# Kernel tuning notes

Hardware: AMD Instinct MI355X
Metric: run time of the kernel (lower is better)

The kernel has to match this reference:

```python
import jax, jax.numpy as jnp
import numpy as np

N_NODES = 50000
N_EDGES = 800000
IN_DIM = 128
OUT_DIM = 128


def setup_inputs() -> dict:
    key = jax.random.key(0)
    k1, k2, k3, k4, k5 = jax.random.split(key, 5)
    x = jax.random.normal(k1, (N_NODES, IN_DIM), dtype=jnp.float32)
    # Xavier-uniform-ish scale for the two weight matrices
    scale = float(np.sqrt(6.0 / (IN_DIM + OUT_DIM)))
    Wg = jax.random.uniform(k2, (OUT_DIM, IN_DIM), dtype=jnp.float32, minval=-scale, maxval=scale)
    Wl = jax.random.uniform(k3, (OUT_DIM, IN_DIM), dtype=jnp.float32, minval=-scale, maxval=scale)
    bias = jnp.zeros((OUT_DIM,), dtype=jnp.float32)
    neigh_idx = jax.random.randint(k4, (N_EDGES,), 0, N_NODES, dtype=jnp.int32)
    seg_ids = jnp.sort(jax.random.randint(k5, (N_EDGES,), 0, N_NODES, dtype=jnp.int32))
    return {"x": x, "Wg": Wg, "Wl": Wl, "bias": bias,
            "neigh_idx": neigh_idx, "seg_ids": seg_ids}


def reference(x, Wg, Wl, bias, neigh_idx, seg_ids):
    N = x.shape[0]
    # global 1x1 map on all nodes (self path)
    global_maps = x @ Wg.T                                  # [N, out]
    # per-edge neighbor features: local + global maps of the neighbor
    neigh_x = x[neigh_idx]                                  # [E, in]
    mixed = neigh_x @ Wl.T + global_maps[neigh_idx]         # [E, out]
    # segment-mean over each destination node's neighbors
    sums = jax.ops.segment_sum(mixed, seg_ids, num_segments=N)            # [N, out]
    cnt = jax.ops.segment_sum(jnp.ones((seg_ids.shape[0],), x.dtype), seg_ids, num_segments=N)  # [N]
    mean = sums / jnp.maximum(cnt, 1.0)[:, None]
    # deg == 0 nodes: neigh_agg falls back to global_maps (as in the torch loop)
    neigh_agg = jnp.where((cnt > 0)[:, None], mean, global_maps)
    out = neigh_agg + global_maps + bias
    return jax.nn.elu(out)
```

## Files before the change

kernel.cpp:

```cpp
#include <hip/hip_runtime.h>
#include <hip/hip_bf16.h>

#define NN 50000
#define NE 800000
#define DIM 128
#define NTILES (NN / 16)
#define GEMM_BLOCKS 784

#define XF8_BLOCKS 3125
#define OFF_BLOCKS 196
#define V_BLOCKS 128

typedef float f32x4 __attribute__((ext_vector_type(4)));
typedef float f32x2 __attribute__((ext_vector_type(2)));
typedef int   i32x2 __attribute__((ext_vector_type(2)));
typedef __bf16 bf16x8 __attribute__((ext_vector_type(8)));

static __device__ __forceinline__ unsigned short bfbits(float f) {
    __bf16 b = (__bf16)f; return __builtin_bit_cast(unsigned short, b);
}

__global__ void __launch_bounds__(256) prep(const float* __restrict__ x,
        const float* __restrict__ Wg, const float* __restrict__ Wl,
        const int* __restrict__ seg,
        unsigned char* __restrict__ xf8, int* __restrict__ off,
        __bf16* __restrict__ V) {
    int b = blockIdx.x;
    int t = threadIdx.x;
    if (b < XF8_BLOCKS) {
        int i = b * 256 + t;
        const float* p = x + (size_t)i * 8;
        f32x4 v0 = *reinterpret_cast<const f32x4*>(p);
        f32x4 v1 = *reinterpret_cast<const f32x4*>(p + 4);
        int lo = __builtin_amdgcn_cvt_pk_fp8_f32(v0[0], v0[1], 0, false);
        lo     = __builtin_amdgcn_cvt_pk_fp8_f32(v0[2], v0[3], lo, true);
        int hi = __builtin_amdgcn_cvt_pk_fp8_f32(v1[0], v1[1], 0, false);
        hi     = __builtin_amdgcn_cvt_pk_fp8_f32(v1[2], v1[3], hi, true);
        i32x2 o = {lo, hi};
        *reinterpret_cast<i32x2*>(xf8 + (size_t)i * 8) = o;
    } else if (b < XF8_BLOCKS + OFF_BLOCKS) {
        int n = (b - XF8_BLOCKS) * 256 + t;
        if (n <= NN) {
            int lo = 0, hi = NE;
            while (lo < hi) {
                int mid = (lo + hi) >> 1;
                if (seg[mid] < n) lo = mid + 1; else hi = mid;
            }
            off[n] = lo;
        }
    } else {
        int i = (b - XF8_BLOCKS - OFF_BLOCKS) * 256 + t;
        int d = i >> 8;
        int k = i & 255;
        float v;
        if (k < DIM) v = Wg[d * DIM + k];
        else         v = Wg[d * DIM + (k - DIM)] + Wl[d * DIM + (k - DIM)];
        V[i] = (__bf16)v;
    }
}

__global__ void __launch_bounds__(256) seg_mean(const unsigned char* __restrict__ xf8,
        const int* __restrict__ nidx, const int* __restrict__ off,
        int* __restrict__ cnt_ws, __bf16* __restrict__ meanb) {
    int n = blockIdx.x * 4 + (threadIdx.x >> 6);
    if (n >= NN) return;
    int lane = threadIdx.x & 63;
    int s = off[n], e = off[n + 1];
    const unsigned short* xu = reinterpret_cast<const unsigned short*>(xf8);
    float a0 = 0.f, a1 = 0.f, b0 = 0.f, b1 = 0.f;
    int i = s;
    for (; i + 8 <= e; i += 8) {
        unsigned short u0 = xu[nidx[i]   * 64 + lane];
        unsigned short u1 = xu[nidx[i+1] * 64 + lane];
        unsigned short u2 = xu[nidx[i+2] * 64 + lane];
        unsigned short u3 = xu[nidx[i+3] * 64 + lane];
        unsigned short u4 = xu[nidx[i+4] * 64 + lane];
        unsigned short u5 = xu[nidx[i+5] * 64 + lane];
        unsigned short u6 = xu[nidx[i+6] * 64 + lane];
        unsigned short u7 = xu[nidx[i+7] * 64 + lane];
        f32x2 f0 = __builtin_amdgcn_cvt_pk_f32_fp8((int)u0, false);
        f32x2 f1 = __builtin_amdgcn_cvt_pk_f32_fp8((int)u1, false);
        f32x2 f2 = __builtin_amdgcn_cvt_pk_f32_fp8((int)u2, false);
        f32x2 f3 = __builtin_amdgcn_cvt_pk_f32_fp8((int)u3, false);
        f32x2 f4 = __builtin_amdgcn_cvt_pk_f32_fp8((int)u4, false);
        f32x2 f5 = __builtin_amdgcn_cvt_pk_f32_fp8((int)u5, false);
        f32x2 f6 = __builtin_amdgcn_cvt_pk_f32_fp8((int)u6, false);
        f32x2 f7 = __builtin_amdgcn_cvt_pk_f32_fp8((int)u7, false);
        a0 += f0[0] + f2[0]; a1 += f0[1] + f2[1];
        b0 += f1[0] + f3[0]; b1 += f1[1] + f3[1];
        a0 += f4[0] + f6[0]; a1 += f4[1] + f6[1];
        b0 += f5[0] + f7[0]; b1 += f5[1] + f7[1];
    }
    for (; i + 4 <= e; i += 4) {
        unsigned short u0 = xu[nidx[i]   * 64 + lane];
        unsigned short u1 = xu[nidx[i+1] * 64 + lane];
        unsigned short u2 = xu[nidx[i+2] * 64 + lane];
        unsigned short u3 = xu[nidx[i+3] * 64 + lane];
        f32x2 f0 = __builtin_amdgcn_cvt_pk_f32_fp8((int)u0, false);
        f32x2 f1 = __builtin_amdgcn_cvt_pk_f32_fp8((int)u1, false);
        f32x2 f2 = __builtin_amdgcn_cvt_pk_f32_fp8((int)u2, false);
        f32x2 f3 = __builtin_amdgcn_cvt_pk_f32_fp8((int)u3, false);
        a0 += f0[0] + f2[0]; a1 += f0[1] + f2[1];
        b0 += f1[0] + f3[0]; b1 += f1[1] + f3[1];
    }
    for (; i < e; ++i) {
        unsigned short u = xu[nidx[i] * 64 + lane];
        f32x2 f = __builtin_amdgcn_cvt_pk_f32_fp8((int)u, false);
        a0 += f[0]; a1 += f[1];
    }
    float s0 = a0 + b0, s1 = a1 + b1;
    int c = e - s;
    float inv = c > 0 ? 1.f / (float)c : 0.f;
    unsigned o = (unsigned)bfbits(s0 * inv) | ((unsigned)bfbits(s1 * inv) << 16);
    reinterpret_cast<unsigned*>(meanb)[n * 64 + lane] = o;
    if (lane == 0) cnt_ws[n] = c;
}

__global__ void __launch_bounds__(256) gemm_ep(const float* __restrict__ x,
        const __bf16* __restrict__ meanb, const __bf16* __restrict__ V,
        const float* __restrict__ bias, const int* __restrict__ cnt_ws,
        float* __restrict__ out) {
    int tid = threadIdx.x;
    int w = tid >> 6;
    int lane = tid & 63;
    int rowin = lane & 15;
    int kg = lane >> 4;
    int rbase = kg * 4;

    bf16x8 Bf[8][2];
    #pragma unroll
    for (int s = 0; s < 8; ++s)
        #pragma unroll
        for (int ff = 0; ff < 2; ++ff) {
            int d = (w * 2 + ff) * 16 + rowin;
            Bf[s][ff] = *reinterpret_cast<const bf16x8*>(&V[d * 256 + s * 32 + kg * 8]);
        }
    float bs0 = bias[(w * 2) * 16 + rowin];
    float bs1 = bias[(w * 2 + 1) * 16 + rowin];

    for (int t = blockIdx.x; t < NTILES; t += gridDim.x) {
        int m0 = t * 16;
        int row = m0 + rowin;
        f32x4 acc0 = {}, acc1 = {};
        #pragma unroll
        for (int s = 0; s < 4; ++s) {
            const float* xp = x + (size_t)row * DIM + s * 32 + kg * 8;
            f32x4 v0 = *reinterpret_cast<const f32x4*>(xp);
            f32x4 v1 = *reinterpret_cast<const f32x4*>(xp + 4);
            bf16x8 a;
            a[0]=(__bf16)v0[0]; a[1]=(__bf16)v0[1]; a[2]=(__bf16)v0[2]; a[3]=(__bf16)v0[3];
            a[4]=(__bf16)v1[0]; a[5]=(__bf16)v1[1]; a[6]=(__bf16)v1[2]; a[7]=(__bf16)v1[3];
            acc0 = __builtin_amdgcn_mfma_f32_16x16x32_bf16(a, Bf[s][0], acc0, 0, 0, 0);
            acc1 = __builtin_amdgcn_mfma_f32_16x16x32_bf16(a, Bf[s][1], acc1, 0, 0, 0);
        }
        #pragma unroll
        for (int s = 0; s < 4; ++s) {
            bf16x8 a = *reinterpret_cast<const bf16x8*>(&meanb[row * DIM + s * 32 + kg * 8]);
            acc0 = __builtin_amdgcn_mfma_f32_16x16x32_bf16(a, Bf[s + 4][0], acc0, 0, 0, 0);
            acc1 = __builtin_amdgcn_mfma_f32_16x16x32_bf16(a, Bf[s + 4][1], acc1, 0, 0, 0);
        }
        #pragma unroll
        for (int r = 0; r < 4; ++r) {
            int n = m0 + rbase + r;
            int c = cnt_ws[n];
            float v0 = acc0[r];
            float z0 = v0 + (c == 0 ? v0 : 0.f) + bs0;
            out[n * DIM + (w * 2) * 16 + rowin] = z0 > 0.f ? z0 : expm1f(z0);
            float v1 = acc1[r];
            float z1 = v1 + (c == 0 ? v1 : 0.f) + bs1;
            out[n * DIM + (w * 2 + 1) * 16 + rowin] = z1 > 0.f ? z1 : expm1f(z1);
        }
    }
}

extern "C" void kernel_launch(void* const* d_in, const int* in_sizes, int n_in,
                              void* d_out, int out_size, void* d_ws, size_t ws_size,
                              hipStream_t stream) {
    const float* x    = (const float*)d_in[0];
    const float* Wg   = (const float*)d_in[1];
    const float* Wl   = (const float*)d_in[2];
    const float* bias = (const float*)d_in[3];
    const int*   nidx = (const int*)d_in[4];
    const int*   seg  = (const int*)d_in[5];
    float* out = (float*)d_out;

    char* p = (char*)d_ws;
    __bf16* V = (__bf16*)p;           p += DIM * 256 * 2;
    int* off = (int*)p;               p += (((NN + 1) * 4) + 511) & ~511ull;
    int* cnt = (int*)p;               p += ((NN * 4) + 511) & ~511ull;
    __bf16* meanb = (__bf16*)p;       p += (size_t)NN * DIM * 2;
    unsigned char* xf8 = (unsigned char*)p;

    prep     <<<XF8_BLOCKS + OFF_BLOCKS + V_BLOCKS, 256, 0, stream>>>(x, Wg, Wl, seg, xf8, off, V);
    seg_mean <<<(NN + 3) / 4, 256, 0, stream>>>(xf8, nidx, off, cnt, meanb);
    gemm_ep  <<<GEMM_BLOCKS, 256, 0, stream>>>(x, meanb, V, bias, cnt, out);
}
```

Baseline: 150.4 us.

## Fuse segment-mean gather into GEMM epilogue kernel via LDS tile

Merges the seg_mean and gemm_ep kernels into one kernel with one 16-row tile per block. Each wave gathers and averages four nodes' fp8 neighbor rows into a shared-memory bf16 tile, then the block runs the MFMA GEMM against that tile. This drops the global round trip of the bf16 mean and count arrays and one kernel launch. In exchange the GEMM no longer uses a persistent grid, and every block reloads the weight fragments from global memory and serializes its gather before its MFMA work.

Result: no change. 153.3 us (+2.0%).

```diff
diff --git a/kernel.cpp b/kernel.cpp
--- a/kernel.cpp
+++ b/kernel.cpp
@@ -4,8 +4,7 @@
 #define NN 50000
 #define NE 800000
 #define DIM 128
-#define NTILES (NN / 16)
-#define GEMM_BLOCKS 784
+#define NT (NN / 16)
 
 #define XF8_BLOCKS 3125
 #define OFF_BLOCKS 196
@@ -59,73 +58,78 @@
     }
 }
 
-__global__ void __launch_bounds__(256) seg_mean(const unsigned char* __restrict__ xf8,
-        const int* __restrict__ nidx, const int* __restrict__ off,
-        int* __restrict__ cnt_ws, __bf16* __restrict__ meanb) {
-    int n = blockIdx.x * 4 + (threadIdx.x >> 6);
-    if (n >= NN) return;
-    int lane = threadIdx.x & 63;
-    int s = off[n], e = off[n + 1];
-    const unsigned short* xu = reinterpret_cast<const unsigned short*>(xf8);
-    float a0 = 0.f, a1 = 0.f, b0 = 0.f, b1 = 0.f;
-    int i = s;
-    for (; i + 8 <= e; i += 8) {
-        unsigned short u0 = xu[nidx[i]   * 64 + lane];
-        unsigned short u1 = xu[nidx[i+1] * 64 + lane];
-        unsigned short u2 = xu[nidx[i+2] * 64 + lane];
-        unsigned short u3 = xu[nidx[i+3] * 64 + lane];
-        unsigned short u4 = xu[nidx[i+4] * 64 + lane];
-        unsigned short u5 = xu[nidx[i+5] * 64 + lane];
-        unsigned short u6 = xu[nidx[i+6] * 64 + lane];
-        unsigned short u7 = xu[nidx[i+7] * 64 + lane];
-        f32x2 f0 = __builtin_amdgcn_cvt_pk_f32_fp8((int)u0, false);
-        f32x2 f1 = __builtin_amdgcn_cvt_pk_f32_fp8((int)u1, false);
-        f32x2 f2 = __builtin_amdgcn_cvt_pk_f32_fp8((int)u2, false);
-        f32x2 f3 = __builtin_amdgcn_cvt_pk_f32_fp8((int)u3, false);
-        f32x2 f4 = __builtin_amdgcn_cvt_pk_f32_fp8((int)u4, false);
-        f32x2 f5 = __builtin_amdgcn_cvt_pk_f32_fp8((int)u5, false);
-        f32x2 f6 = __builtin_amdgcn_cvt_pk_f32_fp8((int)u6, false);
-        f32x2 f7 = __builtin_amdgcn_cvt_pk_f32_fp8((int)u7, false);
-        a0 += f0[0] + f2[0]; a1 += f0[1] + f2[1];
-        b0 += f1[0] + f3[0]; b1 += f1[1] + f3[1];
-        a0 += f4[0] + f6[0]; a1 += f4[1] + f6[1];
-        b0 += f5[0] + f7[0]; b1 += f5[1] + f7[1];
-    }
-    for (; i + 4 <= e; i += 4) {
-        unsigned short u0 = xu[nidx[i]   * 64 + lane];
-        unsigned short u1 = xu[nidx[i+1] * 64 + lane];
-        unsigned short u2 = xu[nidx[i+2] * 64 + lane];
-        unsigned short u3 = xu[nidx[i+3] * 64 + lane];
-        f32x2 f0 = __builtin_amdgcn_cvt_pk_f32_fp8((int)u0, false);
-        f32x2 f1 = __builtin_amdgcn_cvt_pk_f32_fp8((int)u1, false);
-        f32x2 f2 = __builtin_amdgcn_cvt_pk_f32_fp8((int)u2, false);
-        f32x2 f3 = __builtin_amdgcn_cvt_pk_f32_fp8((int)u3, false);
-        a0 += f0[0] + f2[0]; a1 += f0[1] + f2[1];
-        b0 += f1[0] + f3[0]; b1 += f1[1] + f3[1];
-    }
-    for (; i < e; ++i) {
-        unsigned short u = xu[nidx[i] * 64 + lane];
-        f32x2 f = __builtin_amdgcn_cvt_pk_f32_fp8((int)u, false);
-        a0 += f[0]; a1 += f[1];
-    }
-    float s0 = a0 + b0, s1 = a1 + b1;
-    int c = e - s;
-    float inv = c > 0 ? 1.f / (float)c : 0.f;
-    unsigned o = (unsigned)bfbits(s0 * inv) | ((unsigned)bfbits(s1 * inv) << 16);
-    reinterpret_cast<unsigned*>(meanb)[n * 64 + lane] = o;
-    if (lane == 0) cnt_ws[n] = c;
-}
-
-__global__ void __launch_bounds__(256) gemm_ep(const float* __restrict__ x,
-        const __bf16* __restrict__ meanb, const __bf16* __restrict__ V,
-        const float* __restrict__ bias, const int* __restrict__ cnt_ws,
-        float* __restrict__ out) {
+__global__ void __launch_bounds__(256) fused(const float* __restrict__ x,
+        const unsigned char* __restrict__ xf8, const __bf16* __restrict__ V,
+        const float* __restrict__ bias, const int* __restrict__ nidx,
+        const int* __restrict__ off, float* __restrict__ out) {
+    __shared__ __bf16 mean_lds[16 * 136];
+    __shared__ int off_lds[17];
+    __shared__ int cnt_lds[16];
+
     int tid = threadIdx.x;
     int w = tid >> 6;
     int lane = tid & 63;
     int rowin = lane & 15;
     int kg = lane >> 4;
-    int rbase = kg * 4;
+    int m0 = blockIdx.x * 16;
+
+    if (tid < 17) off_lds[tid] = off[m0 + tid];
+    __syncthreads();
+
+    const unsigned short* xu = reinterpret_cast<const unsigned short*>(xf8);
+
+    #pragma unroll
+    for (int j = 0; j < 4; ++j) {
+        int r = w * 4 + j;
+        int s = off_lds[r], e = off_lds[r + 1];
+        float a0 = 0.f, a1 = 0.f, b0 = 0.f, b1 = 0.f;
+        int i = s;
+        for (; i + 8 <= e; i += 8) {
+            unsigned short u0 = xu[nidx[i]   * 64 + lane];
+            unsigned short u1 = xu[nidx[i+1] * 64 + lane];
+            unsigned short u2 = xu[nidx[i+2] * 64 + lane];
+            unsigned short u3 = xu[nidx[i+3] * 64 + lane];
+            unsigned short u4 = xu[nidx[i+4] * 64 + lane];
+            unsigned short u5 = xu[nidx[i+5] * 64 + lane];
+            unsigned short u6 = xu[nidx[i+6] * 64 + lane];
+            unsigned short u7 = xu[nidx[i+7] * 64 + lane];
+            f32x2 f0 = __builtin_amdgcn_cvt_pk_f32_fp8((int)u0, false);
+            f32x2 f1 = __builtin_amdgcn_cvt_pk_f32_fp8((int)u1, false);
+            f32x2 f2 = __builtin_amdgcn_cvt_pk_f32_fp8((int)u2, false);
+            f32x2 f3 = __builtin_amdgcn_cvt_pk_f32_fp8((int)u3, false);
+            f32x2 f4 = __builtin_amdgcn_cvt_pk_f32_fp8((int)u4, false);
+            f32x2 f5 = __builtin_amdgcn_cvt_pk_f32_fp8((int)u5, false);
+            f32x2 f6 = __builtin_amdgcn_cvt_pk_f32_fp8((int)u6, false);
+            f32x2 f7 = __builtin_amdgcn_cvt_pk_f32_fp8((int)u7, false);
+            a0 += f0[0] + f2[0]; a1 += f0[1] + f2[1];
+            b0 += f1[0] + f3[0]; b1 += f1[1] + f3[1];
+            a0 += f4[0] + f6[0]; a1 += f4[1] + f6[1];
+            b0 += f5[0] + f7[0]; b1 += f5[1] + f7[1];
+        }
+        for (; i + 4 <= e; i += 4) {
+            unsigned short u0 = xu[nidx[i]   * 64 + lane];
+            unsigned short u1 = xu[nidx[i+1] * 64 + lane];
+            unsigned short u2 = xu[nidx[i+2] * 64 + lane];
+            unsigned short u3 = xu[nidx[i+3] * 64 + lane];
+            f32x2 f0 = __builtin_amdgcn_cvt_pk_f32_fp8((int)u0, false);
+            f32x2 f1 = __builtin_amdgcn_cvt_pk_f32_fp8((int)u1, false);
+            f32x2 f2 = __builtin_amdgcn_cvt_pk_f32_fp8((int)u2, false);
+            f32x2 f3 = __builtin_amdgcn_cvt_pk_f32_fp8((int)u3, false);
+            a0 += f0[0] + f2[0]; a1 += f0[1] + f2[1];
+            b0 += f1[0] + f3[0]; b1 += f1[1] + f3[1];
+        }
+        for (; i < e; ++i) {
+            unsigned short u = xu[nidx[i] * 64 + lane];
+            f32x2 f = __builtin_amdgcn_cvt_pk_f32_fp8((int)u, false);
+            a0 += f[0]; a1 += f[1];
+        }
+        int c = e - s;
+        float inv = c > 0 ? 1.f / (float)c : 0.f;
+        unsigned o = (unsigned)bfbits((a0 + b0) * inv)
+                   | ((unsigned)bfbits((a1 + b1) * inv) << 16);
+        *reinterpret_cast<unsigned*>(&mean_lds[r * 136 + lane * 2]) = o;
+        if (lane == 0) cnt_lds[r] = c;
+    }
 
     bf16x8 Bf[8][2];
     #pragma unroll
@@ -138,10 +142,9 @@
     float bs0 = bias[(w * 2) * 16 + rowin];
     float bs1 = bias[(w * 2 + 1) * 16 + rowin];
 
-    for (int t = blockIdx.x; t < NTILES; t += gridDim.x) {
-        int m0 = t * 16;
+    bf16x8 axs[4];
+    {
         int row = m0 + rowin;
-        f32x4 acc0 = {}, acc1 = {};
         #pragma unroll
         for (int s = 0; s < 4; ++s) {
             const float* xp = x + (size_t)row * DIM + s * 32 + kg * 8;
@@ -150,26 +153,37 @@
             bf16x8 a;
             a[0]=(__bf16)v0[0]; a[1]=(__bf16)v0[1]; a[2]=(__bf16)v0[2]; a[3]=(__bf16)v0[3];
             a[4]=(__bf16)v1[0]; a[5]=(__bf16)v1[1]; a[6]=(__bf16)v1[2]; a[7]=(__bf16)v1[3];
-            acc0 = __builtin_amdgcn_mfma_f32_16x16x32_bf16(a, Bf[s][0], acc0, 0, 0, 0);
-            acc1 = __builtin_amdgcn_mfma_f32_16x16x32_bf16(a, Bf[s][1], acc1, 0, 0, 0);
-        }
-        #pragma unroll
-        for (int s = 0; s < 4; ++s) {
-            bf16x8 a = *reinterpret_cast<const bf16x8*>(&meanb[row * DIM + s * 32 + kg * 8]);
-            acc0 = __builtin_amdgcn_mfma_f32_16x16x32_bf16(a, Bf[s + 4][0], acc0, 0, 0, 0);
-            acc1 = __builtin_amdgcn_mfma_f32_16x16x32_bf16(a, Bf[s + 4][1], acc1, 0, 0, 0);
-        }
-        #pragma unroll
-        for (int r = 0; r < 4; ++r) {
-            int n = m0 + rbase + r;
-            int c = cnt_ws[n];
-            float v0 = acc0[r];
-            float z0 = v0 + (c == 0 ? v0 : 0.f) + bs0;
-            out[n * DIM + (w * 2) * 16 + rowin] = z0 > 0.f ? z0 : expm1f(z0);
-            float v1 = acc1[r];
-            float z1 = v1 + (c == 0 ? v1 : 0.f) + bs1;
-            out[n * DIM + (w * 2 + 1) * 16 + rowin] = z1 > 0.f ? z1 : expm1f(z1);
-        }
+            axs[s] = a;
+        }
+    }
+
+    __syncthreads();
+
+    f32x4 acc0 = {}, acc1 = {};
+    #pragma unroll
+    for (int s = 0; s < 4; ++s) {
+        acc0 = __builtin_amdgcn_mfma_f32_16x16x32_bf16(axs[s], Bf[s][0], acc0, 0, 0, 0);
+        acc1 = __builtin_amdgcn_mfma_f32_16x16x32_bf16(axs[s], Bf[s][1], acc1, 0, 0, 0);
+    }
+    #pragma unroll
+    for (int s = 0; s < 4; ++s) {
+        bf16x8 a = *reinterpret_cast<const bf16x8*>(&mean_lds[rowin * 136 + s * 32 + kg * 8]);
+        acc0 = __builtin_amdgcn_mfma_f32_16x16x32_bf16(a, Bf[s + 4][0], acc0, 0, 0, 0);
+        acc1 = __builtin_amdgcn_mfma_f32_16x16x32_bf16(a, Bf[s + 4][1], acc1, 0, 0, 0);
+    }
+
+    int rbase = kg * 4;
+    #pragma unroll
+    for (int r = 0; r < 4; ++r) {
+        int rr = rbase + r;
+        int n = m0 + rr;
+        int c = cnt_lds[rr];
+        float v0 = acc0[r];
+        float z0 = v0 + (c == 0 ? v0 : 0.f) + bs0;
+        out[n * DIM + (w * 2) * 16 + rowin] = z0 > 0.f ? z0 : expm1f(z0);
+        float v1 = acc1[r];
+        float z1 = v1 + (c == 0 ? v1 : 0.f) + bs1;
+        out[n * DIM + (w * 2 + 1) * 16 + rowin] = z1 > 0.f ? z1 : expm1f(z1);
     }
 }
 
@@ -187,11 +201,8 @@
     char* p = (char*)d_ws;
     __bf16* V = (__bf16*)p;           p += DIM * 256 * 2;
     int* off = (int*)p;               p += (((NN + 1) * 4) + 511) & ~511ull;
-    int* cnt = (int*)p;               p += ((NN * 4) + 511) & ~511ull;
-    __bf16* meanb = (__bf16*)p;       p += (size_t)NN * DIM * 2;
     unsigned char* xf8 = (unsigned char*)p;
 
-    prep     <<<XF8_BLOCKS + OFF_BLOCKS + V_BLOCKS, 256, 0, stream>>>(x, Wg, Wl, seg, xf8, off, V);
-    seg_mean <<<(NN + 3) / 4, 256, 0, stream>>>(xf8, nidx, off, cnt, meanb);
-    gemm_ep  <<<GEMM_BLOCKS, 256, 0, stream>>>(x, meanb, V, bias, cnt, out);
-}
+    prep  <<<XF8_BLOCKS + OFF_BLOCKS + V_BLOCKS, 256, 0, stream>>>(x, Wg, Wl, seg, xf8, off, V);
+    fused <<<NT, 256, 0, stream>>>(x, xf8, V, bias, nidx, off, out);
+}
```
